# Kernel optimization log

Hardware: AMD Instinct MI355X
Metric: run time of the kernel (lower is better)

## Reference

```python
import jax, jax.numpy as jnp
import numpy as np

N, F_IN, F_OUT, HEADS = 4096, 128, 64, 4


def setup_inputs() -> dict:
    key = jax.random.key(0)
    k1, k2, k3, k4, k5 = jax.random.split(key, 5)
    X = jax.random.normal(k1, (N, F_IN), dtype=jnp.float32)
    A = jax.random.randint(k2, (N, N), 0, 2, dtype=jnp.int32)
    # zero the diagonal: the torch loop always prepends the self node, so the
    # adjacency must not also contain it (would duplicate the self term).
    A = A * (1 - jnp.eye(N, dtype=jnp.int32))
    # per-head Linear(F_IN, F_OUT) weights/bias and Linear(2*F_OUT, 1, bias=False)
    W = jax.random.normal(k3, (HEADS, F_OUT, F_IN), dtype=jnp.float32) / np.sqrt(F_IN)
    b = jax.random.normal(k4, (HEADS, F_OUT), dtype=jnp.float32) * 0.02
    att = jax.random.normal(k5, (HEADS, 2 * F_OUT), dtype=jnp.float32) / np.sqrt(2 * F_OUT)
    return {"X": X, "A": A, "W": W, "b": b, "att": att}


def reference(X, A, W, b, att):
    # H[h, n, o] = line_h(X)
    H = jnp.einsum('nf,hof->hno', X, W) + b[:, None, :]
    f_out = W.shape[1]
    a_src, a_dst = att[:, :f_out], att[:, f_out:]
    # score e_ij = leaky_relu(a_src.H_i + a_dst.H_j)
    s = jnp.einsum('hno,ho->hn', H, a_src)  # query-side term (xi_bar expanded)
    d = jnp.einsum('hno,ho->hn', H, a_dst)  # neighbor-side term
    e = jax.nn.leaky_relu(s[:, :, None] + d[:, None, :])  # [H, N, N]
    # neighbor set = {self} U {j : A_ij != 0}
    mask = (A > 0) | jnp.eye(A.shape[0], dtype=bool)
    e = jnp.where(mask[None], e, -jnp.inf)
    alpha = jax.nn.softmax(e, axis=-1)  # segment softmax per node row
    # weighted sum per head, then mean over heads (sum / head in the original)
    out = jnp.einsum('hnm,hmo->no', alpha, H) / W.shape[0]
    return out  # [N, F_OUT]
```

## Files before the change

kernel.cpp:

```cpp
#include <hip/hip_runtime.h>
#include <hip/hip_bf16.h>


#define NN 4096
#define FIN 128
#define FOUT 64
#define NH 4

typedef __attribute__((ext_vector_type(8))) short bf16x8;
typedef __attribute__((ext_vector_type(4))) float f32x4;
typedef __attribute__((ext_vector_type(4))) unsigned int u32x4;

__device__ __forceinline__ unsigned short f32_bf16(float f) {
    unsigned u = __builtin_bit_cast(unsigned, f);
    u += 0x7fffu + ((u >> 16) & 1u);
    return (unsigned short)(u >> 16);
}

__global__ __launch_bounds__(256) void zero_f4(float4* __restrict__ p, int n4) {
    int i = blockIdx.x * 256 + threadIdx.x;
    if (i < n4) p[i] = make_float4(0.f, 0.f, 0.f, 0.f);
}

__global__ __launch_bounds__(256) void pack_bits(
    const int* __restrict__ A, unsigned long long* __restrict__ Abits)
{
    const int b    = blockIdx.x;
    const int row  = b >> 4;
    const int c0   = (b & 15) * 256;
    const int lane = threadIdx.x & 63;
    const int wv   = threadIdx.x >> 6;
    const int col  = c0 + wv * 64 + lane;
    unsigned long long m = __ballot(A[(size_t)row * NN + col] > 0);
    if (lane == 0) Abits[(size_t)row * 64 + (c0 >> 6) + wv] = m;
}

__global__ __launch_bounds__(256) void gat_prep(
    const float* __restrict__ X, const float* __restrict__ W,
    const float* __restrict__ b, const float* __restrict__ att,
    unsigned short* __restrict__ HbfT, float* __restrict__ Hrow,
    float* __restrict__ s_out, float* __restrict__ d_out,
    float* __restrict__ es_g, float* __restrict__ es2_g,
    float* __restrict__ ed_g, float* __restrict__ ed2_g)
{
    const int rb = blockIdx.x;
    const int h  = blockIdx.y;
    const int n0 = rb * 32;
    const int t  = threadIdx.x;

    __shared__ float Xl[32][132];
    __shared__ float Wt[128][68];

    for (int g = t; g < 32 * 32; g += 256) {
        int row = g >> 5, c4 = g & 31;
        float4 v = *(const float4*)&X[(size_t)(n0 + row) * FIN + c4 * 4];
        *(float4*)&Xl[row][c4 * 4] = v;
    }
    for (int g = t; g < 64 * 32; g += 256) {
        int o = g >> 5, c4 = g & 31;
        float4 v = *(const float4*)&W[((size_t)h * FOUT + o) * FIN + c4 * 4];
        Wt[c4 * 4 + 0][o] = v.x; Wt[c4 * 4 + 1][o] = v.y;
        Wt[c4 * 4 + 2][o] = v.z; Wt[c4 * 4 + 3][o] = v.w;
    }
    __syncthreads();

    const int rg = t >> 4;
    const int og = t & 15;
    float acc[2][4] = {};

    #pragma unroll 4
    for (int f4 = 0; f4 < 32; ++f4) {
        float xv[2][4], wv[4][4];
        #pragma unroll
        for (int i = 0; i < 2; ++i) {
            float4 tmp = *(const float4*)&Xl[rg * 2 + i][f4 * 4];
            xv[i][0] = tmp.x; xv[i][1] = tmp.y; xv[i][2] = tmp.z; xv[i][3] = tmp.w;
        }
        #pragma unroll
        for (int k = 0; k < 4; ++k) {
            float4 tmp = *(const float4*)&Wt[f4 * 4 + k][og * 4];
            wv[k][0] = tmp.x; wv[k][1] = tmp.y; wv[k][2] = tmp.z; wv[k][3] = tmp.w;
        }
        #pragma unroll
        for (int i = 0; i < 2; ++i)
            #pragma unroll
            for (int k = 0; k < 4; ++k)
                #pragma unroll
                for (int jj = 0; jj < 4; ++jj)
                    acc[i][jj] = fmaf(xv[i][k], wv[k][jj], acc[i][jj]);
    }

    float bb[4], as_[4], ad_[4];
    #pragma unroll
    for (int jj = 0; jj < 4; ++jj) {
        bb[jj]  = b[h * FOUT + og * 4 + jj];
        as_[jj] = att[h * 2 * FOUT + og * 4 + jj];
        ad_[jj] = att[h * 2 * FOUT + FOUT + og * 4 + jj];
    }
    #pragma unroll
    for (int i = 0; i < 2; ++i)
        #pragma unroll
        for (int jj = 0; jj < 4; ++jj)
            acc[i][jj] += bb[jj];

    float sp[2] = {0.f, 0.f}, dp[2] = {0.f, 0.f};
    #pragma unroll
    for (int i = 0; i < 2; ++i)
        #pragma unroll
        for (int jj = 0; jj < 4; ++jj) {
            sp[i] = fmaf(acc[i][jj], as_[jj], sp[i]);
            dp[i] = fmaf(acc[i][jj], ad_[jj], dp[i]);
        }
    #pragma unroll
    for (int off = 1; off < 16; off <<= 1) {
        #pragma unroll
        for (int i = 0; i < 2; ++i) {
            sp[i] += __shfl_xor(sp[i], off);
            dp[i] += __shfl_xor(dp[i], off);
        }
    }
    if (og == 0) {
        #pragma unroll
        for (int i = 0; i < 2; ++i) {
            int nn = n0 + rg * 2 + i;
            s_out[h * NN + nn]  = sp[i];
            d_out[h * NN + nn]  = dp[i];
            es_g [h * NN + nn]  = __expf(sp[i]);
            es2_g[h * NN + nn]  = __expf(0.01f * sp[i]);
            ed_g [h * NN + nn]  = __expf(dp[i]);
            ed2_g[h * NN + nn]  = __expf(0.01f * dp[i]);
        }
    }

    #pragma unroll
    for (int i = 0; i < 2; ++i) {
        float4 v = make_float4(acc[i][0], acc[i][1], acc[i][2], acc[i][3]);
        *(float4*)&Hrow[((size_t)h * NN + n0 + rg * 2 + i) * FOUT + og * 4] = v;
    }
    #pragma unroll
    for (int jj = 0; jj < 4; ++jj) {
        int o = og * 4 + jj;
        ushort2 p;
        p.x = f32_bf16(acc[0][jj]);
        p.y = f32_bf16(acc[1][jj]);
        *(ushort2*)&HbfT[((size_t)h * FOUT + o) * NN + n0 + rg * 2] = p;
    }
}

__global__ __launch_bounds__(512, 4) void gat_main(
    const unsigned* __restrict__ Abits, const unsigned short* __restrict__ HbfT,
    const float* __restrict__ es_g, const float* __restrict__ es2_g,
    const float* __restrict__ ed_g, const float* __restrict__ ed2_g,
    float* __restrict__ Hacc, float* __restrict__ lpart)
{
    const int n0 = blockIdx.x * 128;
    const int c0 = blockIdx.y * 256;
    const int hg = blockIdx.z;
    const int tid  = threadIdx.x;
    const int w    = tid >> 6;
    const int lane = tid & 63;
    const int r    = lane & 15;
    const int q    = lane >> 4;

    __shared__ unsigned short Hlds[2][64][256];
    __shared__ unsigned bits_lds[128 * 9];

    #pragma unroll
    for (int it = 0; it < 8; ++it) {
        int flat = it * 512 + tid;
        int rowc = flat >> 5;
        int c16  = flat & 31;
        int o    = rowc & 63, hl2 = rowc >> 6;
        int blk  = c16 ^ (o & 31);
        *(bf16x8*)&Hlds[hl2][o][blk * 8] =
            *(const bf16x8*)&HbfT[((size_t)(hg * 2 + hl2) * FOUT + o) * NN + c0 + c16 * 8];
    }
    #pragma unroll
    for (int it = 0; it < 2; ++it) {
        int flat = it * 512 + tid;
        int row = flat >> 3, wd = flat & 7;
        bits_lds[row * 9 + wd] = Abits[(size_t)(n0 + row) * 128 + (c0 >> 5) + wd];
    }
    __syncthreads();

    bf16x8 ones;
    #pragma unroll
    for (int i = 0; i < 8; ++i) ones[i] = (short)0x3F80;

    const int bits_base = (w * 16 + r) * 9;
    const int qs = q * 8;

    for (int hl = 0; hl < 2; ++hl) {
        const int h  = hg * 2 + hl;
        const int n  = n0 + w * 16 + r;
        const float es  = es_g [h * NN + n];
        const float es2 = es2_g[h * NN + n];
        const float* edh  = ed_g  + h * NN + c0;
        const float* ed2h = ed2_g + h * NN + c0;

        f32x4 acc0 = {0,0,0,0}, acc1 = {0,0,0,0}, acc2 = {0,0,0,0},
              acc3 = {0,0,0,0}, accl = {0,0,0,0};

        #pragma unroll
        for (int step = 0; step < 8; ++step) {
            const unsigned bits32 = bits_lds[bits_base + step];
            const int mk = step * 32 + qs;

            const float4 e0 = *(const float4*)&edh [mk];
            const float4 e1 = *(const float4*)&edh [mk + 4];
            const float4 g0 = *(const float4*)&ed2h[mk];
            const float4 g1 = *(const float4*)&ed2h[mk + 4];
            const float edv [8] = {e0.x, e0.y, e0.z, e0.w, e1.x, e1.y, e1.z, e1.w};
            const float ed2v[8] = {g0.x, g0.y, g0.z, g0.w, g1.x, g1.y, g1.z, g1.w};

            u32x4 afu;
            #pragma unroll
            for (int p = 0; p < 4; ++p) {
                const int j0 = 2 * p, j1 = 2 * p + 1;
                float wa = ((bits32 >> (qs + j0)) & 1u)
                         ? fmaxf(es * edv[j0], es2 * ed2v[j0]) : 0.0f;
                float wb = ((bits32 >> (qs + j1)) & 1u)
                         ? fmaxf(es * edv[j1], es2 * ed2v[j1]) : 0.0f;
                afu[p] = (unsigned)f32_bf16(wa) | ((unsigned)f32_bf16(wb) << 16);
            }
            const bf16x8 af = __builtin_bit_cast(bf16x8, afu);

            const int mb = step * 4 + q;
            const bf16x8 b0 = *(const bf16x8*)&Hlds[hl][r     ][(mb ^ ((r     ) & 31)) * 8];
            const bf16x8 b1 = *(const bf16x8*)&Hlds[hl][r + 16][(mb ^ ((r + 16) & 31)) * 8];
            const bf16x8 b2 = *(const bf16x8*)&Hlds[hl][r + 32][(mb ^ ((r + 32) & 31)) * 8];
            const bf16x8 b3 = *(const bf16x8*)&Hlds[hl][r + 48][(mb ^ ((r + 48) & 31)) * 8];

            acc0 = __builtin_amdgcn_mfma_f32_16x16x32_bf16(af, b0,   acc0, 0, 0, 0);
            acc1 = __builtin_amdgcn_mfma_f32_16x16x32_bf16(af, b1,   acc1, 0, 0, 0);
            acc2 = __builtin_amdgcn_mfma_f32_16x16x32_bf16(af, b2,   acc2, 0, 0, 0);
            acc3 = __builtin_amdgcn_mfma_f32_16x16x32_bf16(af, b3,   acc3, 0, 0, 0);
            accl = __builtin_amdgcn_mfma_f32_16x16x32_bf16(af, ones, accl, 0, 0, 0);
        }

        float* hb = Hacc + ((size_t)h * NN + n0 + w * 16) * FOUT;
        #pragma unroll
        for (int reg = 0; reg < 4; ++reg) {
            const int rr = q * 4 + reg;
            atomicAdd(&hb[rr * FOUT +  0 + r], acc0[reg]);
            atomicAdd(&hb[rr * FOUT + 16 + r], acc1[reg]);
            atomicAdd(&hb[rr * FOUT + 32 + r], acc2[reg]);
            atomicAdd(&hb[rr * FOUT + 48 + r], acc3[reg]);
        }
        if (r == 0) {
            #pragma unroll
            for (int reg = 0; reg < 4; ++reg)
                atomicAdd(&lpart[h * NN + n0 + w * 16 + q * 4 + reg], accl[reg]);
        }
    }
}

__global__ __launch_bounds__(256) void gat_fin(
    const float* __restrict__ Hacc, const float* __restrict__ Hrow,
    const float* __restrict__ lpart, const float* __restrict__ s_g,
    const float* __restrict__ d_g, float* __restrict__ out)
{
    const int tid = threadIdx.x;
    const int rr  = tid >> 4;
    const int c4  = tid & 15;
    const int n   = blockIdx.x * 16 + rr;
    const int o   = c4 * 4;

    float4 res = make_float4(0.f, 0.f, 0.f, 0.f);
    #pragma unroll
    for (int h = 0; h < NH; ++h) {
        float l  = lpart[h * NN + n];
        float tt = s_g[h * NN + n] + d_g[h * NN + n];
        float wd = __expf(fmaxf(tt, 0.01f * tt));
        float inv = 0.25f / (l + wd);
        float4 ha = *(const float4*)&Hacc[((size_t)h * NN + n) * FOUT + o];
        float4 hr = *(const float4*)&Hrow[((size_t)h * NN + n) * FOUT + o];
        res.x += (ha.x + wd * hr.x) * inv;
        res.y += (ha.y + wd * hr.y) * inv;
        res.z += (ha.z + wd * hr.z) * inv;
        res.w += (ha.w + wd * hr.w) * inv;
    }
    *(float4*)&out[(size_t)n * FOUT + o] = res;
}

extern "C" void kernel_launch(void* const* d_in, const int* in_sizes, int n_in,
                              void* d_out, int out_size, void* d_ws, size_t ws_size,
                              hipStream_t stream) {
    const float* X   = (const float*)d_in[0];
    const int*   A   = (const int*)  d_in[1];
    const float* W   = (const float*)d_in[2];
    const float* b   = (const float*)d_in[3];
    const float* att = (const float*)d_in[4];
    float* out = (float*)d_out;

    char* ws = (char*)d_ws;
    unsigned short* HbfT = (unsigned short*)ws;
    size_t off = (size_t)NH * FOUT * NN * 2;
    float* s_buf = (float*)(ws + off);  off += (size_t)NH * NN * 4;
    float* d_buf = (float*)(ws + off);  off += (size_t)NH * NN * 4;
    float* Hacc  = (float*)(ws + off);  off += (size_t)NH * NN * FOUT * 4;
    float* lpart = (float*)(ws + off);  off += (size_t)NH * NN * 4;
    float* Hrow  = (float*)(ws + off);  off += (size_t)NH * NN * FOUT * 4;
    unsigned long long* Abits = (unsigned long long*)(ws + off);
    off += (size_t)NN * 64 * 8;
    float* es_buf  = (float*)(ws + off); off += (size_t)NH * NN * 4;
    float* es2_buf = (float*)(ws + off); off += (size_t)NH * NN * 4;
    float* ed_buf  = (float*)(ws + off); off += (size_t)NH * NN * 4;
    float* ed2_buf = (float*)(ws + off); off += (size_t)NH * NN * 4;

    const int n4 = (NH * NN * FOUT + NH * NN) / 4;
    zero_f4<<<(n4 + 255) / 256, 256, 0, stream>>>((float4*)Hacc, n4);
    pack_bits<<<NN * 16, 256, 0, stream>>>(A, Abits);
    gat_prep<<<dim3(128, 4), 256, 0, stream>>>(X, W, b, att, HbfT, Hrow, s_buf, d_buf,
                                               es_buf, es2_buf, ed_buf, ed2_buf);
    gat_main<<<dim3(32, 16, 2), 512, 0, stream>>>((const unsigned*)Abits, HbfT,
                                                  es_buf, es2_buf, ed_buf, ed2_buf,
                                                  Hacc, lpart);
    gat_fin<<<256, 256, 0, stream>>>(Hacc, Hrow, lpart, s_buf, d_buf, out);
}
```

Before: 195.8 us.

## Restructure gat_main to one head per block looping over two column chunks

Each block now handles a single head and loops over two 256-column chunks, keeping its accumulators in registers across chunks. This halves the number of atomicAdd flushes to Hacc/lpart, halves LDS use for the H tile, and raises the occupancy hint to 8 blocks per CU. The trade-off is that the adjacency bits are reloaded per head instead of being shared by two heads, and there is an extra sync between chunks. The bf16 packing also moves to the intrinsic conversion with simpler bit tests.

```diff
diff --git a/kernel.cpp b/kernel.cpp
--- a/kernel.cpp
+++ b/kernel.cpp
@@ -147,63 +147,64 @@
     }
 }
 
-__global__ __launch_bounds__(512, 4) void gat_main(
+__global__ __launch_bounds__(512, 8) void gat_main(
     const unsigned* __restrict__ Abits, const unsigned short* __restrict__ HbfT,
     const float* __restrict__ es_g, const float* __restrict__ es2_g,
     const float* __restrict__ ed_g, const float* __restrict__ ed2_g,
     float* __restrict__ Hacc, float* __restrict__ lpart)
 {
     const int n0 = blockIdx.x * 128;
-    const int c0 = blockIdx.y * 256;
-    const int hg = blockIdx.z;
+    const int cg = blockIdx.y;
+    const int h  = blockIdx.z;
     const int tid  = threadIdx.x;
     const int w    = tid >> 6;
     const int lane = tid & 63;
     const int r    = lane & 15;
     const int q    = lane >> 4;
 
-    __shared__ unsigned short Hlds[2][64][256];
+    __shared__ unsigned short Hlds[64][256];
     __shared__ unsigned bits_lds[128 * 9];
 
-    #pragma unroll
-    for (int it = 0; it < 8; ++it) {
-        int flat = it * 512 + tid;
-        int rowc = flat >> 5;
-        int c16  = flat & 31;
-        int o    = rowc & 63, hl2 = rowc >> 6;
-        int blk  = c16 ^ (o & 31);
-        *(bf16x8*)&Hlds[hl2][o][blk * 8] =
-            *(const bf16x8*)&HbfT[((size_t)(hg * 2 + hl2) * FOUT + o) * NN + c0 + c16 * 8];
-    }
-    #pragma unroll
-    for (int it = 0; it < 2; ++it) {
-        int flat = it * 512 + tid;
-        int row = flat >> 3, wd = flat & 7;
-        bits_lds[row * 9 + wd] = Abits[(size_t)(n0 + row) * 128 + (c0 >> 5) + wd];
-    }
-    __syncthreads();
-
-    bf16x8 ones;
-    #pragma unroll
-    for (int i = 0; i < 8; ++i) ones[i] = (short)0x3F80;
-
+    const int n  = n0 + w * 16 + r;
+    const float es  = es_g [h * NN + n];
+    const float es2 = es2_g[h * NN + n];
     const int bits_base = (w * 16 + r) * 9;
     const int qs = q * 8;
 
-    for (int hl = 0; hl < 2; ++hl) {
-        const int h  = hg * 2 + hl;
-        const int n  = n0 + w * 16 + r;
-        const float es  = es_g [h * NN + n];
-        const float es2 = es2_g[h * NN + n];
+    bf16x8 ones;
+    #pragma unroll
+    for (int i = 0; i < 8; ++i) ones[i] = (short)0x3F80;
+
+    f32x4 acc0 = {0,0,0,0}, acc1 = {0,0,0,0}, acc2 = {0,0,0,0},
+          acc3 = {0,0,0,0}, accl = {0,0,0,0};
+
+    for (int ch = 0; ch < 2; ++ch) {
+        const int c0 = cg * 512 + ch * 256;
+        __syncthreads();
+
+        #pragma unroll
+        for (int it = 0; it < 4; ++it) {
+            int flat = it * 512 + tid;
+            int o    = flat >> 5;
+            int c16  = flat & 31;
+            int blk  = c16 ^ (o & 31);
+            *(bf16x8*)&Hlds[o][blk * 8] =
+                *(const bf16x8*)&HbfT[((size_t)h * FOUT + o) * NN + c0 + c16 * 8];
+        }
+        #pragma unroll
+        for (int it = 0; it < 2; ++it) {
+            int flat = it * 512 + tid;
+            int row = flat >> 3, wd = flat & 7;
+            bits_lds[row * 9 + wd] = Abits[(size_t)(n0 + row) * 128 + (c0 >> 5) + wd];
+        }
+        __syncthreads();
+
         const float* edh  = ed_g  + h * NN + c0;
         const float* ed2h = ed2_g + h * NN + c0;
 
-        f32x4 acc0 = {0,0,0,0}, acc1 = {0,0,0,0}, acc2 = {0,0,0,0},
-              acc3 = {0,0,0,0}, accl = {0,0,0,0};
-
         #pragma unroll
         for (int step = 0; step < 8; ++step) {
-            const unsigned bits32 = bits_lds[bits_base + step];
+            const unsigned bits8 = bits_lds[bits_base + step] >> qs;
             const int mk = step * 32 + qs;
 
             const float4 e0 = *(const float4*)&edh [mk];
@@ -217,19 +218,22 @@
             #pragma unroll
             for (int p = 0; p < 4; ++p) {
                 const int j0 = 2 * p, j1 = 2 * p + 1;
-                float wa = ((bits32 >> (qs + j0)) & 1u)
+                float wa = (bits8 & (1u << j0))
                          ? fmaxf(es * edv[j0], es2 * ed2v[j0]) : 0.0f;
-                float wb = ((bits32 >> (qs + j1)) & 1u)
+                float wb = (bits8 & (1u << j1))
                          ? fmaxf(es * edv[j1], es2 * ed2v[j1]) : 0.0f;
-                afu[p] = (unsigned)f32_bf16(wa) | ((unsigned)f32_bf16(wb) << 16);
+                __hip_bfloat162 pk = __float22bfloat162_rn(make_float2(wa, wb));
+                unsigned u;
+                __builtin_memcpy(&u, &pk, sizeof(u));
+                afu[p] = u;
             }
             const bf16x8 af = __builtin_bit_cast(bf16x8, afu);
 
             const int mb = step * 4 + q;
-            const bf16x8 b0 = *(const bf16x8*)&Hlds[hl][r     ][(mb ^ ((r     ) & 31)) * 8];
-            const bf16x8 b1 = *(const bf16x8*)&Hlds[hl][r + 16][(mb ^ ((r + 16) & 31)) * 8];
-            const bf16x8 b2 = *(const bf16x8*)&Hlds[hl][r + 32][(mb ^ ((r + 32) & 31)) * 8];
-            const bf16x8 b3 = *(const bf16x8*)&Hlds[hl][r + 48][(mb ^ ((r + 48) & 31)) * 8];
+            const bf16x8 b0 = *(const bf16x8*)&Hlds[r     ][(mb ^ ((r     ) & 31)) * 8];
+            const bf16x8 b1 = *(const bf16x8*)&Hlds[r + 16][(mb ^ ((r + 16) & 31)) * 8];
+            const bf16x8 b2 = *(const bf16x8*)&Hlds[r + 32][(mb ^ ((r + 32) & 31)) * 8];
+            const bf16x8 b3 = *(const bf16x8*)&Hlds[r + 48][(mb ^ ((r + 48) & 31)) * 8];
 
             acc0 = __builtin_amdgcn_mfma_f32_16x16x32_bf16(af, b0,   acc0, 0, 0, 0);
             acc1 = __builtin_amdgcn_mfma_f32_16x16x32_bf16(af, b1,   acc1, 0, 0, 0);
@@ -237,21 +241,21 @@
             acc3 = __builtin_amdgcn_mfma_f32_16x16x32_bf16(af, b3,   acc3, 0, 0, 0);
             accl = __builtin_amdgcn_mfma_f32_16x16x32_bf16(af, ones, accl, 0, 0, 0);
         }
-
-        float* hb = Hacc + ((size_t)h * NN + n0 + w * 16) * FOUT;
-        #pragma unroll
-        for (int reg = 0; reg < 4; ++reg) {
-            const int rr = q * 4 + reg;
-            atomicAdd(&hb[rr * FOUT +  0 + r], acc0[reg]);
-            atomicAdd(&hb[rr * FOUT + 16 + r], acc1[reg]);
-            atomicAdd(&hb[rr * FOUT + 32 + r], acc2[reg]);
-            atomicAdd(&hb[rr * FOUT + 48 + r], acc3[reg]);
-        }
-        if (r == 0) {
-            #pragma unroll
-            for (int reg = 0; reg < 4; ++reg)
-                atomicAdd(&lpart[h * NN + n0 + w * 16 + q * 4 + reg], accl[reg]);
-        }
+    }
+
+    float* hb = Hacc + ((size_t)h * NN + n0 + w * 16) * FOUT;
+    #pragma unroll
+    for (int reg = 0; reg < 4; ++reg) {
+        const int rr = q * 4 + reg;
+        atomicAdd(&hb[rr * FOUT +  0 + r], acc0[reg]);
+        atomicAdd(&hb[rr * FOUT + 16 + r], acc1[reg]);
+        atomicAdd(&hb[rr * FOUT + 32 + r], acc2[reg]);
+        atomicAdd(&hb[rr * FOUT + 48 + r], acc3[reg]);
+    }
+    if (r == 0) {
+        #pragma unroll
+        for (int reg = 0; reg < 4; ++reg)
+            atomicAdd(&lpart[h * NN + n0 + w * 16 + q * 4 + reg], accl[reg]);
     }
 }
 
@@ -313,8 +317,8 @@
     pack_bits<<<NN * 16, 256, 0, stream>>>(A, Abits);
     gat_prep<<<dim3(128, 4), 256, 0, stream>>>(X, W, b, att, HbfT, Hrow, s_buf, d_buf,
                                                es_buf, es2_buf, ed_buf, ed2_buf);
-    gat_main<<<dim3(32, 16, 2), 512, 0, stream>>>((const unsigned*)Abits, HbfT,
-                                                  es_buf, es2_buf, ed_buf, ed2_buf,
-                                                  Hacc, lpart);
+    gat_main<<<dim3(32, 8, 4), 512, 0, stream>>>((const unsigned*)Abits, HbfT,
+                                                 es_buf, es2_buf, ed_buf, ed2_buf,
+                                                 Hacc, lpart);
     gat_fin<<<256, 256, 0, stream>>>(Hacc, Hrow, lpart, s_buf, d_buf, out);
 }
```

New measurement: 205.7 us. +5.0%, slower.
